# Kernel optimization log

Hardware: AMD Instinct MI355X
Metric: run time of the kernel (lower is better)

## Reference

```python
import jax, jax.numpy as jnp
import numpy as np

N_NODES = 100000
N_EDGES = 1600000
D_IN = 128
D_HID = 16
N_CLASSES = 40


def _glorot(key, shape):
    lim = float(np.sqrt(6.0 / (shape[0] + shape[1])))
    return jax.random.uniform(key, shape, jnp.float32, -lim, lim)


def setup_inputs() -> dict:
    key = jax.random.key(0)
    ks = jax.random.split(key, 8)
    x = jax.random.normal(ks[0], (N_NODES, D_IN), dtype=jnp.float32)
    edge_index = jax.random.randint(ks[1], (2, N_EDGES), 0, N_NODES, dtype=jnp.int64)
    return {
        "x": x,
        "edge_index": edge_index,
        # conv1: SAGEConv(D_IN, D_HID): lin_l (on aggregated, with bias), lin_r (on root, no bias)
        "W1l": _glorot(ks[2], (D_IN, D_HID)),
        "b1": jnp.zeros((D_HID,), jnp.float32),
        "W1r": _glorot(ks[3], (D_IN, D_HID)),
        # conv2: SAGEConv(D_HID, N_CLASSES)
        "W2l": _glorot(ks[4], (D_HID, N_CLASSES)),
        "b2": jnp.zeros((N_CLASSES,), jnp.float32),
        "W2r": _glorot(ks[5], (D_HID, N_CLASSES)),
    }


def _sage_conv(x, src, dst, Wl, bl, Wr, num_nodes):
    # mean aggregation of source-node features into destination nodes
    summed = jax.ops.segment_sum(x[src], dst, num_segments=num_nodes)  # [N, D]
    cnt = jax.ops.segment_sum(jnp.ones_like(dst, dtype=x.dtype), dst, num_segments=num_nodes)
    agg = summed / jnp.maximum(cnt, 1.0)[:, None]
    return agg @ Wl + bl + x @ Wr


def reference(x, edge_index, W1l, b1, W1r, W2l, b2, W2r):
    src, dst = edge_index[0], edge_index[1]
    n = x.shape[0]
    h = jax.nn.relu(_sage_conv(x, src, dst, W1l, b1, W1r, n))
    # F.dropout with training=self.training; module evaluated in eval mode -> identity
    out = _sage_conv(h, src, dst, W2l, b2, W2r, n)
    return jax.nn.log_softmax(out, axis=1)
```

## Files before the change

### kernel.cpp

```cpp
#include <hip/hip_runtime.h>
#include <math.h>

typedef _Float16 f16;

constexpr int NN   = 100000;
constexpr int DIN  = 128;
constexpr int DH   = 16;
constexpr int NC   = 40;
constexpr int CAP  = 48;
constexpr int NB   = (NN + 127) / 128;
constexpr int BC   = 2816;
constexpr int BSTR = 16;

static_assert(NN % 8 == 0, "agg grids assume NN % 8 == 0");

template <bool VEC4>
__global__ __launch_bounds__(1024)
void k_part(const int* __restrict__ src, const int* __restrict__ dst, int E,
            int* __restrict__ bcur, int* __restrict__ part)
{
    __shared__ int lh[NB];
    __shared__ int lbase[NB];
    int t = threadIdx.x;
    for (int i = t; i < NB; i += 1024) lh[i] = 0;
    __syncthreads();
    long base = (long)blockIdx.x * 8192;
    int pk[8], bk[8], rk[8];
    if (VEC4 && base + 8192 <= (long)E) {
        const int4* s4 = (const int4*)(src + base) + t * 2;
        const int4* d4 = (const int4*)(dst + base) + t * 2;
        int4 sa = s4[0], sb = s4[1];
        int4 da = d4[0], db = d4[1];
        int ss[8] = {sa.x, sa.y, sa.z, sa.w, sb.x, sb.y, sb.z, sb.w};
        int dd[8] = {da.x, da.y, da.z, da.w, db.x, db.y, db.z, db.w};
        #pragma unroll
        for (int i = 0; i < 8; ++i) {
            bk[i] = dd[i] >> 7;
            pk[i] = (ss[i] << 7) | (dd[i] & 127);
            rk[i] = atomicAdd(&lh[bk[i]], 1);
        }
    } else {
        #pragma unroll
        for (int i = 0; i < 8; ++i) {
            long e = base + (long)t * 8 + i;
            if (e < E) {
                int s = src[e], d = dst[e];
                bk[i] = d >> 7;
                pk[i] = (s << 7) | (d & 127);
                rk[i] = atomicAdd(&lh[bk[i]], 1);
            } else bk[i] = -1;
        }
    }
    __syncthreads();
    for (int i = t; i < NB; i += 1024)
        lbase[i] = lh[i] ? atomicAdd(&bcur[i * BSTR], lh[i]) : 0;
    __syncthreads();
    #pragma unroll
    for (int i = 0; i < 8; ++i) {
        if (bk[i] >= 0) {
            int idx = lbase[bk[i]] + rk[i];
            if (idx < BC) part[(long)bk[i] * BC + idx] = pk[i];
        }
    }
}

__global__ void k_proj(const float* __restrict__ x,
                       const float* __restrict__ W1l, const float* __restrict__ W1r,
                       f16* __restrict__ p1h, float* __restrict__ p1r)
{
    __shared__ float ps[2][64][DH + 1];
    int t  = threadIdx.x;
    int nl = t & 63;
    int halfu = __builtin_amdgcn_readfirstlane((t >> 6) & 1);
    int khu   = __builtin_amdgcn_readfirstlane(t >> 7);
    long n  = (long)blockIdx.x * 64 + nl;
    long ncl = n < NN ? n : NN - 1;
    const float4* xr = (const float4*)(x + ncl * DIN + khu * 64);
    const float*  Wk = (halfu ? W1r : W1l) + khu * 64 * DH;

    float acc[DH];
    #pragma unroll
    for (int j = 0; j < DH; ++j) acc[j] = 0.f;
    #pragma unroll
    for (int k4 = 0; k4 < 16; ++k4) {
        float4 v = xr[k4];
        const float* wr = Wk + k4 * 4 * DH;
        #pragma unroll
        for (int j = 0; j < DH; ++j) {
            acc[j] = fmaf(v.x, wr[j],          acc[j]);
            acc[j] = fmaf(v.y, wr[DH + j],     acc[j]);
            acc[j] = fmaf(v.z, wr[2 * DH + j], acc[j]);
            acc[j] = fmaf(v.w, wr[3 * DH + j], acc[j]);
        }
    }
    if (khu) {
        #pragma unroll
        for (int j = 0; j < DH; ++j) ps[halfu][nl][j] = acc[j];
    }
    __syncthreads();
    if (!khu && n < NN) {
        #pragma unroll
        for (int j = 0; j < DH; ++j) acc[j] += ps[halfu][nl][j];
        if (halfu == 0) {
            union { f16 f[16]; uint4 q[2]; } u;
            #pragma unroll
            for (int j = 0; j < DH; ++j) u.f[j] = (f16)acc[j];
            uint4* po = (uint4*)(p1h + n * DH);
            po[0] = u.q[0]; po[1] = u.q[1];
        } else {
            float4* pr = (float4*)(p1r + n * DH);
            pr[0] = make_float4(acc[0],  acc[1],  acc[2],  acc[3]);
            pr[1] = make_float4(acc[4],  acc[5],  acc[6],  acc[7]);
            pr[2] = make_float4(acc[8],  acc[9],  acc[10], acc[11]);
            pr[3] = make_float4(acc[12], acc[13], acc[14], acc[15]);
        }
    }
}

__global__ __launch_bounds__(512)
void k_ba1(const int* __restrict__ bcur, const int* __restrict__ part,
           const uint4* __restrict__ g4, const float4* __restrict__ p1r4,
           const float* __restrict__ b1,
           int* __restrict__ cnt, int* __restrict__ col, uint4* __restrict__ h4)
{
    __shared__ int scol[128 * CAP];
    __shared__ int cur[128];
    int t = threadIdx.x, b = blockIdx.x;
    if (t < 128) cur[t] = 0;
    __syncthreads();
    long base = (long)b * BC;
    int ne = min(bcur[b * BSTR], BC);
    for (int e = t; e < ne; e += 512) {
        int pk = part[base + e];
        int dl = pk & 127;
        int r  = atomicAdd(&cur[dl], 1);
        if (r < CAP) scol[dl * CAP + r] = pk >> 7;
    }
    __syncthreads();
    if (t < 128) {
        int node = (b << 7) + t;
        if (node < NN) cnt[node] = cur[t];
    }
    int* gcol = col + (long)b * 128 * CAP;
    for (int i = t; i < 128 * CAP; i += 512) gcol[i] = scol[i];

    int nl = t >> 2, dh = (t >> 1) & 1, ng = t & 1;
    int node = (b << 7) + nl;
    int degf = cur[nl];
    int deg  = min(degf, CAP);
    const int* cb = scol + nl * CAP;
    float a[8];
    #pragma unroll
    for (int j = 0; j < 8; ++j) a[j] = 0.f;
    int i = ng;
    for (; i + 6 < deg; i += 8) {
        int s0 = cb[i], s1 = cb[i+2], s2 = cb[i+4], s3 = cb[i+6];
        uint4 v0 = g4[(long)s0*2+dh], v1 = g4[(long)s1*2+dh],
              v2 = g4[(long)s2*2+dh], v3 = g4[(long)s3*2+dh];
        const f16 *p0=(const f16*)&v0, *p1=(const f16*)&v1,
                  *p2=(const f16*)&v2, *p3=(const f16*)&v3;
        #pragma unroll
        for (int j = 0; j < 8; ++j)
            a[j] += (float)p0[j] + (float)p1[j] + (float)p2[j] + (float)p3[j];
    }
    for (; i < deg; i += 2) {
        int s = cb[i];
        uint4 v = g4[(long)s*2+dh];
        const f16* p = (const f16*)&v;
        #pragma unroll
        for (int j = 0; j < 8; ++j) a[j] += (float)p[j];
    }
    #pragma unroll
    for (int j = 0; j < 8; ++j) a[j] += __shfl_xor(a[j], 1);
    if (ng == 0 && node < NN) {
        float inv = 1.0f / fmaxf((float)degf, 1.0f);
        float4 bl = ((const float4*)b1)[dh*2+0];
        float4 bh = ((const float4*)b1)[dh*2+1];
        float4 rl = p1r4[(long)node*4 + dh*2+0];
        float4 rh = p1r4[(long)node*4 + dh*2+1];
        float bb[8] = {bl.x,bl.y,bl.z,bl.w, bh.x,bh.y,bh.z,bh.w};
        float rr[8] = {rl.x,rl.y,rl.z,rl.w, rh.x,rh.y,rh.z,rh.w};
        union { f16 f[8]; uint4 u; } o;
        #pragma unroll
        for (int j = 0; j < 8; ++j)
            o.f[j] = (f16)fmaxf(fmaf(a[j], inv, bb[j] + rr[j]), 0.f);
        h4[(long)node*2+dh] = o.u;
    }
}

__global__ void k_agg2o(const int* __restrict__ cnt, const int* __restrict__ col,
                        const uint4* __restrict__ g4,
                        const float* __restrict__ W2l, const float* __restrict__ b2,
                        const float* __restrict__ W2r, float* __restrict__ out)
{
    __shared__ float sW[2 * DH * NC + NC];
    __shared__ float sA[32][DH + 1];
    __shared__ float sH[32][DH + 1];
    int t = threadIdx.x;
    for (int i = t; i < DH * NC; i += 256) {
        sW[i]           = W2l[i];
        sW[DH * NC + i] = W2r[i];
    }
    if (t < NC) sW[2 * DH * NC + t] = b2[t];

    int lane = t & 63;
    int wv   = (blockIdx.x * 256 + t) >> 6;
    int n    = wv * 8 + (lane >> 3);
    int dh   = (lane >> 2) & 1;
    int ng   = lane & 3;
    int nl2  = t >> 3;
    int degf = cnt[n];
    int deg  = min(degf, CAP);
    const int* cb = col + (long)n * CAP;
    float a[8];
    #pragma unroll
    for (int j = 0; j < 8; ++j) a[j] = 0.f;
    int i = ng;
    for (; i + 12 < deg; i += 16) {
        int s0 = cb[i], s1 = cb[i+4], s2 = cb[i+8], s3 = cb[i+12];
        uint4 v0 = g4[(long)s0*2+dh], v1 = g4[(long)s1*2+dh],
              v2 = g4[(long)s2*2+dh], v3 = g4[(long)s3*2+dh];
        const f16 *p0=(const f16*)&v0, *p1=(const f16*)&v1,
                  *p2=(const f16*)&v2, *p3=(const f16*)&v3;
        #pragma unroll
        for (int j = 0; j < 8; ++j)
            a[j] += (float)p0[j] + (float)p1[j] + (float)p2[j] + (float)p3[j];
    }
    for (; i < deg; i += 4) {
        int s = cb[i];
        uint4 v = g4[(long)s*2+dh];
        const f16* p = (const f16*)&v;
        #pragma unroll
        for (int j = 0; j < 8; ++j) a[j] += (float)p[j];
    }
    #pragma unroll
    for (int j = 0; j < 8; ++j) {
        a[j] += __shfl_xor(a[j], 1);
        a[j] += __shfl_xor(a[j], 2);
    }
    if (ng == 0) {
        float inv = 1.0f / fmaxf((float)degf, 1.0f);
        #pragma unroll
        for (int j = 0; j < 8; ++j) sA[nl2][dh*8+j] = a[j] * inv;
    } else if (ng == 1) {
        uint4 hv4 = g4[(long)n*2+dh];
        const f16* hp = (const f16*)&hv4;
        #pragma unroll
        for (int j = 0; j < 8; ++j) sH[nl2][dh*8+j] = (float)hp[j];
    }
    __syncthreads();

    float av[DH], hv[DH];
    #pragma unroll
    for (int j = 0; j < DH; ++j) { av[j] = sA[nl2][j]; hv[j] = sH[nl2][j]; }
    int lane8 = t & 7;
    float o[5];
    #pragma unroll
    for (int j = 0; j < 5; ++j) {
        int c = lane8 + 8 * j;
        float acc = sW[2 * DH * NC + c];
        #pragma unroll
        for (int k = 0; k < DH; ++k) {
            acc = fmaf(av[k], sW[k * NC + c],           acc);
            acc = fmaf(hv[k], sW[DH * NC + k * NC + c], acc);
        }
        o[j] = acc;
    }
    float mx = o[0];
    #pragma unroll
    for (int j = 1; j < 5; ++j) mx = fmaxf(mx, o[j]);
    #pragma unroll
    for (int m = 1; m <= 4; m <<= 1) mx = fmaxf(mx, __shfl_xor(mx, m));
    float s = 0.f;
    #pragma unroll
    for (int j = 0; j < 5; ++j) s += __expf(o[j] - mx);
    #pragma unroll
    for (int m = 1; m <= 4; m <<= 1) s += __shfl_xor(s, m);
    float lg = mx + __logf(s);
    float* op = out + (long)n * NC;
    #pragma unroll
    for (int j = 0; j < 5; ++j) op[lane8 + 8 * j] = o[j] - lg;
}


extern "C" void kernel_launch(void* const* d_in, const int* in_sizes, int n_in,
                              void* d_out, int out_size, void* d_ws, size_t ws_size,
                              hipStream_t stream) {
    const float* x   = (const float*)d_in[0];
    const int*   ei  = (const int*)d_in[1];
    const float* W1l = (const float*)d_in[2];
    const float* b1  = (const float*)d_in[3];
    const float* W1r = (const float*)d_in[4];
    const float* W2l = (const float*)d_in[5];
    const float* b2  = (const float*)d_in[6];
    const float* W2r = (const float*)d_in[7];
    float* out = (float*)d_out;

    const int E = in_sizes[1] / 2;
    const int* src = ei;
    const int* dst = ei + E;

    int* bcur = (int*)d_ws;
    int* cnt  = bcur + 12544;
    int* col  = cnt + NN;
    int* part = col + (long)NB * 128 * CAP;
    float* p1r = (float*)(part + (long)NB * BC);
    f16*   p1h = (f16*)(p1r + (long)NN * DH);
    f16*   h   = p1h + (long)NN * DH;

    hipMemsetAsync(bcur, 0, NB * BSTR * sizeof(int), stream);

    if ((E & 3) == 0)
        k_part<true ><<<(E + 8191) / 8192, 1024, 0, stream>>>(src, dst, E, bcur, part);
    else
        k_part<false><<<(E + 8191) / 8192, 1024, 0, stream>>>(src, dst, E, bcur, part);

    k_proj <<<(NN + 63) / 64, 256, 0, stream>>>(x, W1l, W1r, p1h, p1r);

    k_ba1  <<<NB, 512, 0, stream>>>(bcur, part, (const uint4*)p1h,
                                    (const float4*)p1r, b1, cnt, col, (uint4*)h);
    k_agg2o<<<(NN + 31) / 32, 256, 0, stream>>>(cnt, col, (const uint4*)h,
                                                W2l, b2, W2r, out);
}
```

Measured before the change: 184.3 us.

## Rebuild layer-2 adjacency in LDS instead of materializing CSR in global memory

Layer 1 no longer writes per-node counts and padded column lists to global memory. A new layer-2 kernel re-bins the partitioned edges into shared memory per 128-node block, then does the gather, the dense projection and log_softmax in the same block. This removes a large global write and read of the padded adjacency. In exchange it repeats the LDS binning and uses fewer lanes per node for the gather.

```diff
diff --git a/kernel.cpp b/kernel.cpp
--- a/kernel.cpp
+++ b/kernel.cpp
@@ -12,7 +12,7 @@
 constexpr int BC   = 2816;
 constexpr int BSTR = 16;
 
-static_assert(NN % 8 == 0, "agg grids assume NN % 8 == 0");
+static_assert(NN % 8 == 0, "grids assume NN % 8 == 0");
 
 template <bool VEC4>
 __global__ __launch_bounds__(1024)
@@ -120,8 +120,7 @@
 __global__ __launch_bounds__(512)
 void k_ba1(const int* __restrict__ bcur, const int* __restrict__ part,
            const uint4* __restrict__ g4, const float4* __restrict__ p1r4,
-           const float* __restrict__ b1,
-           int* __restrict__ cnt, int* __restrict__ col, uint4* __restrict__ h4)
+           const float* __restrict__ b1, uint4* __restrict__ h4)
 {
     __shared__ int scol[128 * CAP];
     __shared__ int cur[128];
@@ -137,12 +136,6 @@
         if (r < CAP) scol[dl * CAP + r] = pk >> 7;
     }
     __syncthreads();
-    if (t < 128) {
-        int node = (b << 7) + t;
-        if (node < NN) cnt[node] = cur[t];
-    }
-    int* gcol = col + (long)b * 128 * CAP;
-    for (int i = t; i < 128 * CAP; i += 512) gcol[i] = scol[i];
 
     int nl = t >> 2, dh = (t >> 1) & 1, ng = t & 1;
     int node = (b << 7) + nl;
@@ -188,98 +181,115 @@
     }
 }
 
-__global__ void k_agg2o(const int* __restrict__ cnt, const int* __restrict__ col,
-                        const uint4* __restrict__ g4,
-                        const float* __restrict__ W2l, const float* __restrict__ b2,
-                        const float* __restrict__ W2r, float* __restrict__ out)
+__global__ __launch_bounds__(512)
+void k_ba2(const int* __restrict__ bcur, const int* __restrict__ part,
+           const uint4* __restrict__ h4,
+           const float* __restrict__ W2l, const float* __restrict__ b2,
+           const float* __restrict__ W2r, float* __restrict__ out)
 {
-    __shared__ float sW[2 * DH * NC + NC];
-    __shared__ float sA[32][DH + 1];
-    __shared__ float sH[32][DH + 1];
-    int t = threadIdx.x;
-    for (int i = t; i < DH * NC; i += 256) {
-        sW[i]           = W2l[i];
-        sW[DH * NC + i] = W2r[i];
-    }
-    if (t < NC) sW[2 * DH * NC + t] = b2[t];
-
-    int lane = t & 63;
-    int wv   = (blockIdx.x * 256 + t) >> 6;
-    int n    = wv * 8 + (lane >> 3);
-    int dh   = (lane >> 2) & 1;
-    int ng   = lane & 3;
-    int nl2  = t >> 3;
-    int degf = cnt[n];
+    __shared__ int scol[128 * CAP];
+    __shared__ int cur[128];
+    int t = threadIdx.x, b = blockIdx.x;
+    if (t < 128) cur[t] = 0;
+    __syncthreads();
+    long base = (long)b * BC;
+    int ne = min(bcur[b * BSTR], BC);
+    for (int e = t; e < ne; e += 512) {
+        int pk = part[base + e];
+        int dl = pk & 127;
+        int r  = atomicAdd(&cur[dl], 1);
+        if (r < CAP) scol[dl * CAP + r] = pk >> 7;
+    }
+    __syncthreads();
+
+    int nl = t >> 2, dh = (t >> 1) & 1, ng = t & 1;
+    int node = (b << 7) + nl;
+    int degf = cur[nl];
     int deg  = min(degf, CAP);
-    const int* cb = col + (long)n * CAP;
+    const int* cb = scol + nl * CAP;
     float a[8];
     #pragma unroll
     for (int j = 0; j < 8; ++j) a[j] = 0.f;
     int i = ng;
-    for (; i + 12 < deg; i += 16) {
-        int s0 = cb[i], s1 = cb[i+4], s2 = cb[i+8], s3 = cb[i+12];
-        uint4 v0 = g4[(long)s0*2+dh], v1 = g4[(long)s1*2+dh],
-              v2 = g4[(long)s2*2+dh], v3 = g4[(long)s3*2+dh];
+    for (; i + 6 < deg; i += 8) {
+        int s0 = cb[i], s1 = cb[i+2], s2 = cb[i+4], s3 = cb[i+6];
+        uint4 v0 = h4[(long)s0*2+dh], v1 = h4[(long)s1*2+dh],
+              v2 = h4[(long)s2*2+dh], v3 = h4[(long)s3*2+dh];
         const f16 *p0=(const f16*)&v0, *p1=(const f16*)&v1,
                   *p2=(const f16*)&v2, *p3=(const f16*)&v3;
         #pragma unroll
         for (int j = 0; j < 8; ++j)
             a[j] += (float)p0[j] + (float)p1[j] + (float)p2[j] + (float)p3[j];
     }
-    for (; i < deg; i += 4) {
+    for (; i < deg; i += 2) {
         int s = cb[i];
-        uint4 v = g4[(long)s*2+dh];
+        uint4 v = h4[(long)s*2+dh];
         const f16* p = (const f16*)&v;
         #pragma unroll
         for (int j = 0; j < 8; ++j) a[j] += (float)p[j];
     }
     #pragma unroll
-    for (int j = 0; j < 8; ++j) {
-        a[j] += __shfl_xor(a[j], 1);
-        a[j] += __shfl_xor(a[j], 2);
-    }
+    for (int j = 0; j < 8; ++j) a[j] += __shfl_xor(a[j], 1);
+    long nodec = node < NN ? (long)node : 0;
+    uint4 rv = h4[nodec*2+dh];
+    __syncthreads();
+
+    float* sA = (float*)scol;
+    float* sH = sA + 128 * 17;
+    float* sW = sH + 128 * 17;
     if (ng == 0) {
         float inv = 1.0f / fmaxf((float)degf, 1.0f);
         #pragma unroll
-        for (int j = 0; j < 8; ++j) sA[nl2][dh*8+j] = a[j] * inv;
-    } else if (ng == 1) {
-        uint4 hv4 = g4[(long)n*2+dh];
-        const f16* hp = (const f16*)&hv4;
-        #pragma unroll
-        for (int j = 0; j < 8; ++j) sH[nl2][dh*8+j] = (float)hp[j];
-    }
-    __syncthreads();
-
-    float av[DH], hv[DH];
-    #pragma unroll
-    for (int j = 0; j < DH; ++j) { av[j] = sA[nl2][j]; hv[j] = sH[nl2][j]; }
-    int lane8 = t & 7;
-    float o[5];
-    #pragma unroll
-    for (int j = 0; j < 5; ++j) {
-        int c = lane8 + 8 * j;
-        float acc = sW[2 * DH * NC + c];
-        #pragma unroll
-        for (int k = 0; k < DH; ++k) {
-            acc = fmaf(av[k], sW[k * NC + c],           acc);
-            acc = fmaf(hv[k], sW[DH * NC + k * NC + c], acc);
-        }
-        o[j] = acc;
-    }
-    float mx = o[0];
-    #pragma unroll
-    for (int j = 1; j < 5; ++j) mx = fmaxf(mx, o[j]);
-    #pragma unroll
-    for (int m = 1; m <= 4; m <<= 1) mx = fmaxf(mx, __shfl_xor(mx, m));
-    float s = 0.f;
-    #pragma unroll
-    for (int j = 0; j < 5; ++j) s += __expf(o[j] - mx);
-    #pragma unroll
-    for (int m = 1; m <= 4; m <<= 1) s += __shfl_xor(s, m);
-    float lg = mx + __logf(s);
-    float* op = out + (long)n * NC;
-    #pragma unroll
-    for (int j = 0; j < 5; ++j) op[lane8 + 8 * j] = o[j] - lg;
+        for (int j = 0; j < 8; ++j) sA[nl*17 + dh*8 + j] = a[j] * inv;
+    } else {
+        const f16* rp = (const f16*)&rv;
+        #pragma unroll
+        for (int j = 0; j < 8; ++j) sH[nl*17 + dh*8 + j] = (float)rp[j];
+    }
+    for (int i2 = t; i2 < DH * NC; i2 += 512) {
+        sW[i2]           = W2l[i2];
+        sW[DH * NC + i2] = W2r[i2];
+    }
+    if (t < NC) sW[2 * DH * NC + t] = b2[t];
+    __syncthreads();
+
+    int l8  = t & 7;
+    int nb0 = t >> 3;
+    #pragma unroll
+    for (int r = 0; r < 2; ++r) {
+        int nl2 = nb0 + (r << 6);
+        int nd  = (b << 7) + nl2;
+        if (nd >= NN) continue;
+        float av[DH], hv[DH];
+        #pragma unroll
+        for (int k = 0; k < DH; ++k) { av[k] = sA[nl2*17 + k]; hv[k] = sH[nl2*17 + k]; }
+        float o[5];
+        #pragma unroll
+        for (int j = 0; j < 5; ++j) {
+            int c = l8 + 8 * j;
+            float acc = sW[2 * DH * NC + c];
+            #pragma unroll
+            for (int k = 0; k < DH; ++k) {
+                acc = fmaf(av[k], sW[k * NC + c],           acc);
+                acc = fmaf(hv[k], sW[DH * NC + k * NC + c], acc);
+            }
+            o[j] = acc;
+        }
+        float mx = o[0];
+        #pragma unroll
+        for (int j = 1; j < 5; ++j) mx = fmaxf(mx, o[j]);
+        #pragma unroll
+        for (int m = 1; m <= 4; m <<= 1) mx = fmaxf(mx, __shfl_xor(mx, m));
+        float s = 0.f;
+        #pragma unroll
+        for (int j = 0; j < 5; ++j) s += __expf(o[j] - mx);
+        #pragma unroll
+        for (int m = 1; m <= 4; m <<= 1) s += __shfl_xor(s, m);
+        float lg = mx + __logf(s);
+        float* op = out + (long)nd * NC;
+        #pragma unroll
+        for (int j = 0; j < 5; ++j) op[l8 + 8 * j] = o[j] - lg;
+    }
 }
 
 
@@ -301,12 +311,10 @@
     const int* dst = ei + E;
 
     int* bcur = (int*)d_ws;
-    int* cnt  = bcur + 12544;
-    int* col  = cnt + NN;
-    int* part = col + (long)NB * 128 * CAP;
+    int* part = bcur + 12544;
     float* p1r = (float*)(part + (long)NB * BC);
     f16*   p1h = (f16*)(p1r + (long)NN * DH);
-    f16*   h   = p1h + (long)NN * DH;
+    f16*   hh  = p1h + (long)NN * DH;
 
     hipMemsetAsync(bcur, 0, NB * BSTR * sizeof(int), stream);
 
@@ -315,10 +323,10 @@
     else
         k_part<false><<<(E + 8191) / 8192, 1024, 0, stream>>>(src, dst, E, bcur, part);
 
-    k_proj <<<(NN + 63) / 64, 256, 0, stream>>>(x, W1l, W1r, p1h, p1r);
-
-    k_ba1  <<<NB, 512, 0, stream>>>(bcur, part, (const uint4*)p1h,
-                                    (const float4*)p1r, b1, cnt, col, (uint4*)h);
-    k_agg2o<<<(NN + 31) / 32, 256, 0, stream>>>(cnt, col, (const uint4*)h,
-                                                W2l, b2, W2r, out);
-}
+    k_proj<<<(NN + 63) / 64, 256, 0, stream>>>(x, W1l, W1r, p1h, p1r);
+
+    k_ba1<<<NB, 512, 0, stream>>>(bcur, part, (const uint4*)p1h,
+                                  (const float4*)p1r, b1, (uint4*)hh);
+    k_ba2<<<NB, 512, 0, stream>>>(bcur, part, (const uint4*)hh,
+                                  W2l, b2, W2r, out);
+}
```

After: 179.3 us. 1.03x faster.
